# Kernel tuning notes

Measured on AMD Instinct MI355X. Metric: run time of the kernel, lower is better.

Reference implementation:

```python
import jax, jax.numpy as jnp
import numpy as np

# dims: C=d_model, DI=expand*C (d_inner), S=d_state, R=dt_rank, K=4 scan dirs
C, DI, S, R, K = 64, 128, 16, 4, 4
Hh, Ww, T, Bsz = 48, 48, 4, 1

def _silu(x):
    return x * jax.nn.sigmoid(x)

def _ln_c(x, w, b, eps=1e-6):
    # LayerNorm2d: normalize over channel dim of [B,C,H,W]
    mu = jnp.mean(x, axis=1, keepdims=True)
    var = jnp.var(x, axis=1, keepdims=True)
    return (x - mu) * jax.lax.rsqrt(var + eps) * w[None, :, None, None] + b[None, :, None, None]

def _cal_kl(cur, prev):
    # elementwise KL over channel-softmax distributions, shape-preserving
    lp = jax.nn.log_softmax(prev, axis=1)
    lq = jax.nn.log_softmax(cur, axis=1)
    return jnp.exp(lp) * (lp - lq)

def _ss2d(x, in_w, in_b, cw, cb, xp_w, dt_w, dt_b, A_logs, Ds, onw, onb, ow, ob):
    # VMamba-style SS2D, channel-first input [B,C,H,W]
    B_, _, H_, W_ = x.shape
    L = H_ * W_
    xz = jnp.einsum('dc,bchw->bdhw', in_w, x) + in_b[None, :, None, None]
    xc, z = jnp.split(xz, 2, axis=1)
    di = xc.shape[1]
    xc = jax.lax.conv_general_dilated(xc, cw[:, None], (1, 1), 'SAME',
        dimension_numbers=('NCHW', 'OIHW', 'NCHW'), feature_group_count=di)
    xc = _silu(xc + cb[None, :, None, None])
    # cross-scan: row-major, col-major, and their reverses -> [B,K,DI,L]
    x1 = xc.reshape(B_, di, L)
    x2 = jnp.swapaxes(xc, 2, 3).reshape(B_, di, L)
    xs = jnp.stack([x1, x2, jnp.flip(x1, -1), jnp.flip(x2, -1)], axis=1)
    xdbl = jnp.einsum('krd,bkdl->bkrl', xp_w, xs)
    dts, Bs, Cs = jnp.split(xdbl, [R, R + S], axis=2)  # [B,K,R,L],[B,K,S,L],[B,K,S,L]
    dt = jax.nn.softplus(jnp.einsum('kdr,bkrl->bkdl', dt_w, dts) + dt_b[None, :, :, None])
    A = -jnp.exp(A_logs)  # [K,DI,S]
    dA = jnp.exp(dt[..., None] * A[None, :, :, None, :])                    # [B,K,DI,L,S]
    dBx = (dt * xs)[..., None] * jnp.swapaxes(Bs, 2, 3)[:, :, None, :, :]   # [B,K,DI,L,S]
    def comb(e1, e2):
        a1, b1 = e1
        a2, b2 = e2
        return (a1 * a2, a2 * b1 + b2)
    _, hs = jax.lax.associative_scan(comb, (dA, dBx), axis=3)
    y = jnp.einsum('bkdls,bksl->bkdl', hs, Cs) + Ds[None, :, :, None] * xs
    # cross-merge back to row-major and sum
    y0 = y[:, 0]
    y1 = jnp.swapaxes(y[:, 1].reshape(B_, di, W_, H_), 2, 3).reshape(B_, di, L)
    y2 = jnp.flip(y[:, 2], -1)
    y3 = jnp.swapaxes(jnp.flip(y[:, 3], -1).reshape(B_, di, W_, H_), 2, 3).reshape(B_, di, L)
    yy = (y0 + y1 + y2 + y3).reshape(B_, di, H_, W_)
    yy = _ln_c(yy, onw, onb) * _silu(z)
    return jnp.einsum('cd,bdhw->bchw', ow, yy) + ob[None, :, None, None]

def setup_inputs():
    key = jax.random.key(0)
    ks = jax.random.split(key, 16)
    rn = lambda k, shp, s: jax.random.normal(k, shp, jnp.float32) * s
    return {
        'image_sequence': rn(ks[0], (Bsz, T, C, Hh, Ww), 1.0),
        'difficult_zone': rn(ks[1], (Bsz, C, Hh, Ww), 1.0),
        'sigma': rn(ks[2], (Bsz, C, Hh, Ww), 0.1),
        # params stacked over the 2 SS2D modules: [0]=mamba_sigma, [1]=mamba_bias
        'in_w': rn(ks[3], (2, 2 * DI, C), C ** -0.5),
        'in_b': rn(ks[4], (2, 2 * DI), 0.02),
        'conv_w': rn(ks[5], (2, DI, 3, 3), 1.0 / 3.0),
        'conv_b': rn(ks[6], (2, DI), 0.02),
        'xp_w': rn(ks[7], (2, K, R + 2 * S, DI), DI ** -0.5),
        'dt_w': rn(ks[8], (2, K, DI, R), R ** -0.5),
        'dt_b': rn(ks[9], (2, K, DI), 0.5),
        'A_logs': jnp.log(1.0 + jax.random.uniform(ks[10], (2, K, DI, S), jnp.float32)),
        'Ds': rn(ks[11], (2, K, DI), 0.5),
        'onw': jnp.ones((2, DI), jnp.float32),
        'onb': jnp.zeros((2, DI), jnp.float32),
        'ow': rn(ks[12], (2, C, DI), 0.02),
        'ob': jnp.zeros((2, C), jnp.float32),
        'niw': jnp.ones((C,), jnp.float32),
        'nib': jnp.zeros((C,), jnp.float32),
        'ndw': jnp.ones((C,), jnp.float32),
        'ndb': jnp.zeros((C,), jnp.float32),
    }

def reference(image_sequence, difficult_zone, sigma, in_w, in_b, conv_w, conv_b, xp_w, dt_w, dt_b, A_logs, Ds, onw, onb, ow, ob, niw, nib, ndw, ndb):
    prev = _ln_c(difficult_zone, ndw, ndb)
    cur = prev * jnp.exp(sigma)  # prev / exp(-sigma)
    for t in range(T):  # strictly sequential recurrence over `length` steps
        s = _ss2d(_cal_kl(cur, prev), in_w[0], in_b[0], conv_w[0], conv_b[0], xp_w[0],
                  dt_w[0], dt_b[0], A_logs[0], Ds[0], onw[0], onb[0], ow[0], ob[0])
        bias = _ss2d(_ln_c(image_sequence[:, t], niw, nib), in_w[1], in_b[1], conv_w[1], conv_b[1], xp_w[1],
                     dt_w[1], dt_b[1], A_logs[1], Ds[1], onw[1], onb[1], ow[1], ob[1])
        cur, prev = cur * jnp.exp(s) + bias, cur
    return cur
```

## Files before the change

kernel.cpp:

```cpp
#include <hip/hip_runtime.h>

#define DEV __device__ __forceinline__

constexpr int Cc = 64, DIc = 128, Sc = 16, Rc = 4, Kc = 4;
constexpr int Lc = 2304, Tc = 4;
constexpr int NCH = 144, CHL = 16;

constexpr int OFF_XCPRE = 0;
constexpr int OFF_Z     = 294912;
constexpr int OFF_XACT  = 589824;
constexpr int OFF_DTS   = 884736;
constexpr int OFF_BS    = 921600;
constexpr int OFF_CS    = 1069056;
constexpr int OFF_Y     = 1216512;
constexpr int OFF_SUMA  = 2396160;
constexpr int OFF_SUMB  = 3575808;
constexpr int OFF_H0    = 4755456;
constexpr int SLOTF     = 5935104;
constexpr int OFF_B1    = 5 * SLOTF;
constexpr int OFF_B2    = OFF_B1 + Lc * Cc;
constexpr int OFF_BIAS  = OFF_B2 + Lc * Cc;
constexpr int OFF_TW    = OFF_BIAS + Tc * Lc * Cc;
constexpr int TW_INW  = 0;
constexpr int TW_XPW  = 32768;
constexpr int TW_OW   = 69632;
constexpr int TW_CW   = 86016;
constexpr int TW_AT   = 88320;
constexpr int TW_DTW  = 104704;

struct Params {
  const float *img, *dz, *sigma, *in_w, *in_b, *conv_w, *conv_b, *xp_w, *dt_w,
              *dt_b, *A_logs, *Ds, *onw, *onb, *ow, *ob, *niw, *nib, *ndw, *ndb;
  float* outp;
  float* ws;
};

DEV float wsum(float v) {
#pragma unroll
  for (int m = 32; m; m >>= 1) v += __shfl_xor(v, m, 64);
  return v;
}
DEV float wmax(float v) {
#pragma unroll
  for (int m = 32; m; m >>= 1) v = fmaxf(v, __shfl_xor(v, m, 64));
  return v;
}
DEV float sigmoidf(float x) { return 1.f / (1.f + __expf(-x)); }
DEV float softplusf(float v) { return (v > 20.f) ? v : __logf(1.f + __expf(v)); }
DEV float fexp2(float x) { return __builtin_amdgcn_exp2f(x); }

DEV int perm_idx(int k, int l) {
  if (k == 0) return l;
  if (k == 1) return (l % 48) * 48 + l / 48;
  if (k == 2) return Lc - 1 - l;
  int pp = Lc - 1 - l;
  return (pp % 48) * 48 + pp / 48;
}

DEV int perm_stride(int k) {
  return (k == 0) ? 1 : (k == 1) ? 48 : (k == 2) ? -1 : -48;
}

__global__ __launch_bounds__(256) void g_transpose(Params p) {
  float* tw = p.ws + OFF_TW;
  int i = blockIdx.x * 256 + threadIdx.x;
  if (i < 32768) {
    int d = i & 255, cc = (i >> 8) & 63, b = i >> 14;
    tw[TW_INW + i] = p.in_w[(b * 256 + d) * 64 + cc];
  }
  if (i < 36864) {
    int kr = i % 144, cc = (i / 144) & 127, b = i / (144 * 128);
    tw[TW_XPW + i] = p.xp_w[(b * 144 + kr) * 128 + cc];
  }
  if (i < 16384) {
    int c = i & 63, d = (i >> 6) & 127, b = i >> 13;
    tw[TW_OW + i] = p.ow[(b * 64 + c) * 128 + d];
  }
  if (i < 2304) {
    int d = i & 127, kk = (i >> 7) % 9, b = i / 1152;
    tw[TW_CW + i] = p.conv_w[(b * 128 + d) * 9 + kk];
  }
  if (i < 16384) {
    int d = i & 127, bks = i >> 7;
    int s = bks & 15, bk = bks >> 4;
    tw[TW_AT + i] = -__expf(p.A_logs[(bk * 128 + d) * 16 + s]) * 1.4426950408889634f;
  }
  if (i < 4096) {
    int d = i & 127, bkr = i >> 7;
    int r = bkr & 3, bk = bkr >> 2;
    tw[TW_DTW + i] = p.dt_w[(bk * 128 + d) * 4 + r];
  }
}

__global__ __launch_bounds__(256) void g_inproj(Params p) {
  __shared__ float xv[8][64];
  int tid = threadIdx.x;
  int slot = blockIdx.y;
  int branch = (slot >= 4) ? 0 : 1;
  float* ws = p.ws;
  float* base = ws + (size_t)slot * SLOTF;
  float* xcpre = base + OFF_XCPRE;
  float* zbuf  = base + OFF_Z;
  const float* wT = ws + OFF_TW + TW_INW + branch * 64 * 256;
  int l0 = blockIdx.x * 8;
  int wv = tid >> 6, c = tid & 63;
#pragma unroll
  for (int q = 0; q < 2; q++) {
    int pp = wv * 2 + q;
    int l = l0 + pp;
    float x;
    if (branch == 1) {
      float v = p.img[(slot * Cc + c) * Lc + l];
      float mu = wsum(v) * (1.f / 64.f);
      float var = wsum(v * v) * (1.f / 64.f) - mu * mu;
      x = (v - mu) * rsqrtf(var + 1e-6f) * p.niw[c] + p.nib[c];
    } else {
      float v = p.dz[c * Lc + l];
      float mu = wsum(v) * (1.f / 64.f);
      float var = wsum(v * v) * (1.f / 64.f) - mu * mu;
      float pv = (v - mu) * rsqrtf(var + 1e-6f) * p.ndw[c] + p.ndb[c];
      float cv = pv * __expf(p.sigma[c * Lc + l]);
      (ws + OFF_B1)[l * Cc + c] = cv;
      float mp = wmax(pv);
      float sp = wsum(__expf(pv - mp));
      float lp = pv - mp - __logf(sp);
      float mq = wmax(cv);
      float sq = wsum(__expf(cv - mq));
      float lq = cv - mq - __logf(sq);
      x = __expf(lp) * (lp - lq);
    }
    xv[pp][c] = x;
  }
  __syncthreads();
  int d = tid;
  float acc[8];
#pragma unroll
  for (int q = 0; q < 8; q++) acc[q] = 0.f;
  for (int cc = 0; cc < Cc; cc++) {
    float wval = wT[cc * 256 + d];
#pragma unroll
    for (int q = 0; q < 8; q++) acc[q] += wval * xv[q][cc];
  }
  float bv = p.in_b[branch * 2 * DIc + d];
  if (d < DIc) {
#pragma unroll
    for (int q = 0; q < 8; q++) xcpre[(l0 + q) * DIc + d] = acc[q] + bv;
  } else {
    int dd = d - DIc;
#pragma unroll
    for (int q = 0; q < 8; q++) zbuf[(l0 + q) * DIc + dd] = acc[q] + bv;
  }
}

__global__ __launch_bounds__(256) void g_conv(Params p, int slot_base) {
  __shared__ float xv[4][DIc];
  int tid = threadIdx.x;
  int slot = slot_base + blockIdx.y;
  int branch = (slot >= 4) ? 0 : 1;
  float* ws = p.ws;
  float* base = ws + (size_t)slot * SLOTF;
  float* xcpre = base + OFF_XCPRE;
  float* xact  = base + OFF_XACT;
  float* dtsb  = base + OFF_DTS;
  float* Bsb   = base + OFF_BS;
  float* Csb   = base + OFF_CS;
  const float* cwT  = ws + OFF_TW + TW_CW + branch * 9 * 128;
  const float* xpwT = ws + OFF_TW + TW_XPW + branch * 128 * 144;
  int h = blockIdx.x / 12;
  int w0 = (blockIdx.x % 12) * 4;
  for (int it = tid; it < 4 * DIc; it += 256) {
    int d = it & (DIc - 1);
    int pp = it >> 7;
    int w = w0 + pp;
    float acc = 0.f;
#pragma unroll
    for (int kh = 0; kh < 3; kh++) {
      int hh = h + kh - 1;
      if ((unsigned)hh < 48u) {
#pragma unroll
        for (int kw = 0; kw < 3; kw++) {
          int wp = w + kw - 1;
          if ((unsigned)wp < 48u)
            acc += cwT[(kh * 3 + kw) * 128 + d] * xcpre[(hh * 48 + wp) * DIc + d];
        }
      }
    }
    float v = acc + p.conv_b[branch * DIc + d];
    float s = v * sigmoidf(v);
    xv[pp][d] = s;
    xact[(h * 48 + w) * DIc + d] = s;
  }
  __syncthreads();
  if (tid < Kc * 36) {
    int k = tid / 36, r = tid % 36;
    float acc[4] = {0.f, 0.f, 0.f, 0.f};
    for (int cc = 0; cc < DIc; cc++) {
      float wvv = xpwT[cc * 144 + tid];
#pragma unroll
      for (int pp = 0; pp < 4; pp++) acc[pp] += wvv * xv[pp][cc];
    }
#pragma unroll
    for (int pp = 0; pp < 4; pp++) {
      int w = w0 + pp;
      int lr = h * 48 + w, lcx = w * 48 + h;
      int pos = (k == 0) ? lr : (k == 1) ? lcx : (k == 2) ? (Lc - 1 - lr) : (Lc - 1 - lcx);
      if (r < Rc) dtsb[(k * Lc + pos) * Rc + r] = acc[pp];
      else if (r < Rc + Sc) Bsb[(k * Lc + pos) * Sc + (r - Rc)] = acc[pp];
      else Csb[(k * Lc + pos) * Sc + (r - Rc - Sc)] = acc[pp];
    }
  }
}

__global__ __launch_bounds__(256, 4) void g_scan1(Params p, int slot_base) {
  __shared__ alignas(16) float2 sDt[CHL][DIc];
  __shared__ alignas(16) float sB[CHL * Sc];
  __shared__ float sCT[2][DIc];
  int tid = threadIdx.x;
  int slot = slot_base + blockIdx.y;
  int branch = (slot >= 4) ? 0 : 1;
  float* ws = p.ws;
  float* base = ws + (size_t)slot * SLOTF;
  const float* xact = base + OFF_XACT;
  const float* Bsb  = base + OFF_BS;
  const float* dtsb = base + OFF_DTS;
  float* sumA = base + OFF_SUMA;
  float* sumB = base + OFF_SUMB;
  int bx = blockIdx.x;
  int k = bx / NCH, ch = bx - k * NCH;
  int d = tid & (DIc - 1);
  int sh = tid >> 7;
  int bk = branch * Kc + k;
  const float* AT   = ws + OFF_TW + TW_AT;
  const float* dtwT = ws + OFF_TW + TW_DTW;
  int l0 = ch * CHL;
  sB[tid] = Bsb[(k * Lc + l0) * Sc + tid];
  float A2[8];
#pragma unroll
  for (int j = 0; j < 8; j++) A2[j] = AT[(bk * 16 + sh * 8 + j) * 128 + d];
  int idx0 = perm_idx(k, l0);
  int st = perm_stride(k);
  float xw[8];
#pragma unroll
  for (int j = 0; j < 8; j++) xw[j] = xact[(idx0 + st * (sh * 8 + j)) * DIc + d];
  float4 dtq[8];
#pragma unroll
  for (int j = 0; j < 8; j++)
    dtq[j] = *(const float4*)(dtsb + (size_t)(k * Lc + l0 + sh * 8 + j) * 4);
  float dw0 = dtwT[(bk * 4 + 0) * 128 + d];
  float dw1 = dtwT[(bk * 4 + 1) * 128 + d];
  float dw2 = dtwT[(bk * 4 + 2) * 128 + d];
  float dw3 = dtwT[(bk * 4 + 3) * 128 + d];
  float db = p.dt_b[bk * DIc + d];
  float ct = 0.f;
#pragma unroll
  for (int j = 0; j < 8; j++) {
    float v = db + dw0 * dtq[j].x + dw1 * dtq[j].y + dw2 * dtq[j].z + dw3 * dtq[j].w;
    float dtv = softplusf(v);
    sDt[sh * 8 + j][d] = make_float2(dtv, dtv * xw[j]);
    ct += dtv;
  }
  sCT[sh][d] = ct;
  __syncthreads();
  float CT = sCT[0][d] + sCT[1][d];
  const float4* B4 = (const float4*)sB;
  float h0 = 0.f, h1 = 0.f, h2 = 0.f, h3 = 0.f, h4 = 0.f, h5 = 0.f, h6 = 0.f, h7 = 0.f;
#pragma unroll
  for (int ib = 0; ib < 4; ib++) {
    float2 dg[4];
    float4 Bg0[4], Bg1[4];
#pragma unroll
    for (int q = 0; q < 4; q++) {
      int i = ib * 4 + q;
      dg[q]  = sDt[i][d];
      Bg0[q] = B4[i * 4 + sh * 2];
      Bg1[q] = B4[i * 4 + sh * 2 + 1];
    }
#pragma unroll
    for (int q = 0; q < 4; q++) {
      float dtv = dg[q].x, dtx = dg[q].y;
#define STEP1(hh, bb, aa2) { float da = fexp2(dtv * (aa2)); hh = da * hh + dtx * (bb); }
      STEP1(h0, Bg0[q].x, A2[0]);
      STEP1(h1, Bg0[q].y, A2[1]);
      STEP1(h2, Bg0[q].z, A2[2]);
      STEP1(h3, Bg0[q].w, A2[3]);
      STEP1(h4, Bg1[q].x, A2[4]);
      STEP1(h5, Bg1[q].y, A2[5]);
      STEP1(h6, Bg1[q].z, A2[6]);
      STEP1(h7, Bg1[q].w, A2[7]);
#undef STEP1
    }
  }
  float* sa = sumA + ((size_t)(k * NCH + ch) * Sc + sh * 8) * DIc + d;
  float* sb = sumB + ((size_t)(k * NCH + ch) * Sc + sh * 8) * DIc + d;
#pragma unroll
  for (int j = 0; j < 8; j++) sa[j * DIc] = fexp2(A2[j] * CT);
  sb[0 * DIc] = h0; sb[1 * DIc] = h1; sb[2 * DIc] = h2; sb[3 * DIc] = h3;
  sb[4 * DIc] = h4; sb[5 * DIc] = h5; sb[6 * DIc] = h6; sb[7 * DIc] = h7;
}

__global__ __launch_bounds__(256) void g_mid(Params p, int slot_base) {
  int gid = blockIdx.x * 256 + threadIdx.x;
  int slot = slot_base + blockIdx.y;
  float* base = p.ws + (size_t)slot * SLOTF;
  const float* sumA = base + OFF_SUMA;
  const float* sumB = base + OFF_SUMB;
  float* h0 = base + OFF_H0;
  int d = gid & (DIc - 1);
  int s = (gid >> 7) & (Sc - 1);
  int k = gid >> 11;
  float h = 0.f;
  for (int g = 0; g < NCH / 16; g++) {
    float a[16], b[16];
#pragma unroll
    for (int j = 0; j < 16; j++) {
      int idx = ((k * NCH + g * 16 + j) * Sc + s) * DIc + d;
      a[j] = sumA[idx];
      b[j] = sumB[idx];
    }
#pragma unroll
    for (int j = 0; j < 16; j++) {
      int idx = ((k * NCH + g * 16 + j) * Sc + s) * DIc + d;
      h0[idx] = h;
      h = a[j] * h + b[j];
    }
  }
}

__global__ __launch_bounds__(512, 4) void g_scan2(Params p, int slot_base) {
  __shared__ alignas(16) float2 sDt[2][CHL][DIc];
  __shared__ alignas(16) float sB[2][CHL * Sc];
  __shared__ alignas(16) float sC[2][CHL * Sc];
  int tid = threadIdx.x;
  int slot = slot_base + blockIdx.y;
  int branch = (slot >= 4) ? 0 : 1;
  float* ws = p.ws;
  float* base = ws + (size_t)slot * SLOTF;
  const float* xact = base + OFF_XACT;
  const float* Bsb  = base + OFF_BS;
  const float* Csb  = base + OFF_CS;
  const float* dtsb = base + OFF_DTS;
  const float* h0b  = base + OFF_H0;
  int pair = blockIdx.x / NCH, chA = blockIdx.x - pair * NCH;
  int d = tid & (DIc - 1);
  int sh = (tid >> 7) & 1;
  int dir = tid >> 8;
  int k = pair + 2 * dir;
  int ch = dir ? (NCH - 1 - chA) : chA;
  int bk = branch * Kc + k;
  float* ypair = base + OFF_Y + (size_t)pair * Lc * DIc;
  const float* AT   = ws + OFF_TW + TW_AT;
  const float* dtwT = ws + OFF_TW + TW_DTW;
  int l0 = ch * CHL;
  int t8 = tid & 255;
  sB[dir][t8] = Bsb[(k * Lc + l0) * Sc + t8];
  sC[dir][t8] = Csb[(k * Lc + l0) * Sc + t8];
  float A2[8];
#pragma unroll
  for (int j = 0; j < 8; j++) A2[j] = AT[(bk * 16 + sh * 8 + j) * 128 + d];
  float hr0, hr1, hr2, hr3, hr4, hr5, hr6, hr7;
  {
    const float* hp = h0b + ((size_t)(k * NCH + ch) * Sc + sh * 8) * DIc + d;
    hr0 = hp[0 * DIc]; hr1 = hp[1 * DIc]; hr2 = hp[2 * DIc]; hr3 = hp[3 * DIc];
    hr4 = hp[4 * DIc]; hr5 = hp[5 * DIc]; hr6 = hp[6 * DIc]; hr7 = hp[7 * DIc];
  }
  int idx0 = perm_idx(k, l0);
  int st = perm_stride(k);
  float xw[8];
#pragma unroll
  for (int j = 0; j < 8; j++) xw[j] = xact[(idx0 + st * (sh * 8 + j)) * DIc + d];
  float4 dtq[8];
#pragma unroll
  for (int j = 0; j < 8; j++)
    dtq[j] = *(const float4*)(dtsb + (size_t)(k * Lc + l0 + sh * 8 + j) * 4);
  float dw0 = dtwT[(bk * 4 + 0) * 128 + d];
  float dw1 = dtwT[(bk * 4 + 1) * 128 + d];
  float dw2 = dtwT[(bk * 4 + 2) * 128 + d];
  float dw3 = dtwT[(bk * 4 + 3) * 128 + d];
  float db = p.dt_b[bk * DIc + d];
  float Dv = p.Ds[bk * DIc + d];
#pragma unroll
  for (int j = 0; j < 8; j++) {
    float v = db + dw0 * dtq[j].x + dw1 * dtq[j].y + dw2 * dtq[j].z + dw3 * dtq[j].w;
    float dtv = softplusf(v);
    sDt[dir][sh * 8 + j][d] = make_float2(dtv, dtv * xw[j]);
  }
  __syncthreads();
  const float4* B4 = (const float4*)sB[dir];
  const float4* C4 = (const float4*)sC[dir];
  float acc[CHL];
#pragma unroll
  for (int ib = 0; ib < 4; ib++) {
    float2 dg[4];
    float4 Bg0[4], Bg1[4];
#pragma unroll
    for (int q = 0; q < 4; q++) {
      int i = ib * 4 + q;
      dg[q]  = sDt[dir][i][d];
      Bg0[q] = B4[i * 4 + sh * 2];
      Bg1[q] = B4[i * 4 + sh * 2 + 1];
    }
#pragma unroll
    for (int q = 0; q < 4; q++) {
      int i = ib * 4 + q;
      float4 Cg0 = C4[i * 4 + sh * 2];
      float4 Cg1 = C4[i * 4 + sh * 2 + 1];
      float dtv = dg[q].x, dtx = dg[q].y;
      float a = 0.f;
#define STEP(hh, bb, cc, aa2) { float da = fexp2(dtv * (aa2)); hh = da * hh + dtx * (bb); a += hh * (cc); }
      STEP(hr0, Bg0[q].x, Cg0.x, A2[0]);
      STEP(hr1, Bg0[q].y, Cg0.y, A2[1]);
      STEP(hr2, Bg0[q].z, Cg0.z, A2[2]);
      STEP(hr3, Bg0[q].w, Cg0.w, A2[3]);
      STEP(hr4, Bg1[q].x, Cg1.x, A2[4]);
      STEP(hr5, Bg1[q].y, Cg1.y, A2[5]);
      STEP(hr6, Bg1[q].z, Cg1.z, A2[6]);
      STEP(hr7, Bg1[q].w, Cg1.w, A2[7]);
#undef STEP
      acc[i] = a;
    }
  }
  if (sh == 0) {
#pragma unroll
    for (int j = 0; j < 8; j++) acc[j] += Dv * xw[j];
  } else {
#pragma unroll
    for (int j = 0; j < 8; j++) acc[8 + j] += Dv * xw[j];
  }
  __syncthreads();
  float* yred = (float*)sDt;
  if (sh == 1) {
#pragma unroll
    for (int i = 0; i < CHL; i++) yred[(dir * CHL + i) * DIc + d] = acc[i];
  }
  __syncthreads();
  if (sh == 0 && dir == 1) {
#pragma unroll
    for (int i = 0; i < CHL; i++) yred[(CHL + i) * DIc + d] += acc[i];
  }
  __syncthreads();
  if (sh == 0 && dir == 0) {
#pragma unroll
    for (int i = 0; i < CHL; i++)
      ypair[(size_t)(idx0 + st * i) * DIc + d] =
          acc[i] + yred[i * DIc + d] + yred[(CHL + (CHL - 1 - i)) * DIc + d];
  }
}

__global__ __launch_bounds__(256) void g_out_bias(Params p) {
  __shared__ float yy[4][DIc];
  __shared__ float ml[4][DIc];
  __shared__ float mnv[4], isv[4];
  int tid = threadIdx.x;
  int slot = blockIdx.y;
  float* ws = p.ws;
  float* base = ws + (size_t)slot * SLOTF;
  const float* y01 = base + OFF_Y;
  const float* y23 = base + OFF_Y + Lc * DIc;
  const float* zb = base + OFF_Z;
  const float* owT = ws + OFF_TW + TW_OW + 128 * 64;
  float* biasb = ws + OFF_BIAS;
  int l0 = blockIdx.x * 4;
  for (int it = tid; it < 4 * DIc; it += 256) {
    int d = it & (DIc - 1), pp = it >> 7;
    size_t off = (size_t)(l0 + pp) * DIc + d;
    yy[pp][d] = y01[off] + y23[off];
  }
  __syncthreads();
  {
    int wv = tid >> 6, c = tid & 63;
    float a = yy[wv][c], b = yy[wv][c + 64];
    float s1 = wsum(a + b);
    float s2 = wsum(a * a + b * b);
    float mu = s1 * (1.f / 128.f);
    float var = s2 * (1.f / 128.f) - mu * mu;
    if (c == 0) { mnv[wv] = mu; isv[wv] = rsqrtf(var + 1e-6f); }
  }
  __syncthreads();
  for (int it = tid; it < 4 * DIc; it += 256) {
    int d = it & (DIc - 1), pp = it >> 7;
    int l = l0 + pp;
    float m = (yy[pp][d] - mnv[pp]) * isv[pp] * p.onw[DIc + d] + p.onb[DIc + d];
    float zv = zb[l * DIc + d];
    ml[pp][d] = m * zv * sigmoidf(zv);
  }
  __syncthreads();
  {
    int pp = tid >> 6, c = tid & 63;
    int l = l0 + pp;
    float acc = p.ob[Cc + c];
    for (int d2 = 0; d2 < DIc; d2++) acc += owT[d2 * 64 + c] * ml[pp][d2];
    biasb[(slot * Lc + l) * Cc + c] = acc;
  }
}

__global__ __launch_bounds__(256) void g_out_s(Params p, int targ, int fuse, int finalw,
                                               const float* curb, float* nxtb) {
  __shared__ float yy[4][DIc];
  __shared__ float ml[4][DIc];
  __shared__ float xvs[4][64];
  __shared__ float mnv[4], isv[4];
  int tid = threadIdx.x;
  float* ws = p.ws;
  float* base = ws + (size_t)4 * SLOTF;
  const float* y01 = base + OFF_Y;
  const float* y23 = base + OFF_Y + Lc * DIc;
  const float* zb = base + OFF_Z;
  float* xcpre = base + OFF_XCPRE;
  float* zbuf  = base + OFF_Z;
  const float* owT  = ws + OFF_TW + TW_OW;
  const float* inwT = ws + OFF_TW + TW_INW;
  const float* biasb = ws + OFF_BIAS;
  int l0 = blockIdx.x * 4;
  for (int it = tid; it < 4 * DIc; it += 256) {
    int d = it & (DIc - 1), pp = it >> 7;
    size_t off = (size_t)(l0 + pp) * DIc + d;
    yy[pp][d] = y01[off] + y23[off];
  }
  __syncthreads();
  {
    int wv = tid >> 6, c = tid & 63;
    float a = yy[wv][c], b = yy[wv][c + 64];
    float s1 = wsum(a + b);
    float s2 = wsum(a * a + b * b);
    float mu = s1 * (1.f / 128.f);
    float var = s2 * (1.f / 128.f) - mu * mu;
    if (c == 0) { mnv[wv] = mu; isv[wv] = rsqrtf(var + 1e-6f); }
  }
  __syncthreads();
  for (int it = tid; it < 4 * DIc; it += 256) {
    int d = it & (DIc - 1), pp = it >> 7;
    int l = l0 + pp;
    float m = (yy[pp][d] - mnv[pp]) * isv[pp] * p.onw[d] + p.onb[d];
    float zv = zb[l * DIc + d];
    ml[pp][d] = m * zv * sigmoidf(zv);
  }
  __syncthreads();
  {
    int pp = tid >> 6, c = tid & 63;
    int l = l0 + pp;
    float acc = p.ob[c];
    for (int d2 = 0; d2 < DIc; d2++) acc += owT[d2 * 64 + c] * ml[pp][d2];
    float cv = curb[l * Cc + c];
    float nv = cv * __expf(acc) + biasb[(targ * Lc + l) * Cc + c];
    nxtb[l * Cc + c] = nv;
    if (finalw) p.outp[c * Lc + l] = nv;
    if (fuse) {
      float mp = wmax(cv);
      float sp = wsum(__expf(cv - mp));
      float lp = cv - mp - __logf(sp);
      float mq = wmax(nv);
      float sq = wsum(__expf(nv - mq));
      float lq = nv - mq - __logf(sq);
      xvs[pp][c] = __expf(lp) * (lp - lq);
    }
  }
  if (fuse) {
    __syncthreads();
    int d = tid;
    float acc[4] = {0.f, 0.f, 0.f, 0.f};
    for (int cc = 0; cc < Cc; cc++) {
      float wval = inwT[cc * 256 + d];
#pragma unroll
      for (int pp = 0; pp < 4; pp++) acc[pp] += wval * xvs[pp][cc];
    }
    float bv = p.in_b[d];
    if (d < DIc) {
#pragma unroll
      for (int pp = 0; pp < 4; pp++) xcpre[(l0 + pp) * DIc + d] = acc[pp] + bv;
    } else {
      int dd = d - DIc;
#pragma unroll
      for (int pp = 0; pp < 4; pp++) zbuf[(l0 + pp) * DIc + dd] = acc[pp] + bv;
    }
  }
}

extern "C" void kernel_launch(void* const* d_in, const int* in_sizes, int n_in,
                              void* d_out, int out_size, void* d_ws, size_t ws_size,
                              hipStream_t stream) {
  (void)in_sizes; (void)n_in; (void)out_size; (void)ws_size;
  Params p;
  p.img    = (const float*)d_in[0];
  p.dz     = (const float*)d_in[1];
  p.sigma  = (const float*)d_in[2];
  p.in_w   = (const float*)d_in[3];
  p.in_b   = (const float*)d_in[4];
  p.conv_w = (const float*)d_in[5];
  p.conv_b = (const float*)d_in[6];
  p.xp_w   = (const float*)d_in[7];
  p.dt_w   = (const float*)d_in[8];
  p.dt_b   = (const float*)d_in[9];
  p.A_logs = (const float*)d_in[10];
  p.Ds     = (const float*)d_in[11];
  p.onw    = (const float*)d_in[12];
  p.onb    = (const float*)d_in[13];
  p.ow     = (const float*)d_in[14];
  p.ob     = (const float*)d_in[15];
  p.niw    = (const float*)d_in[16];
  p.nib    = (const float*)d_in[17];
  p.ndw    = (const float*)d_in[18];
  p.ndb    = (const float*)d_in[19];
  p.outp   = (float*)d_out;
  p.ws     = (float*)d_ws;


  hipLaunchKernelGGL(g_transpose, dim3(144), dim3(256), 0, stream, p);
  hipLaunchKernelGGL(g_inproj, dim3(288, 5), dim3(256), 0, stream, p);
  hipLaunchKernelGGL(g_conv, dim3(576, 5), dim3(256), 0, stream, p, 0);
  hipLaunchKernelGGL(g_scan1, dim3(Kc * NCH, 5), dim3(256), 0, stream, p, 0);
  hipLaunchKernelGGL(g_mid, dim3(32, 5), dim3(256), 0, stream, p, 0);
  hipLaunchKernelGGL(g_scan2, dim3(2 * NCH, 5), dim3(512), 0, stream, p, 0);
  hipLaunchKernelGGL(g_out_bias, dim3(576, 4), dim3(256), 0, stream, p);

  float* b1 = p.ws + OFF_B1;
  float* b2 = p.ws + OFF_B2;
  hipLaunchKernelGGL(g_out_s, dim3(576), dim3(256), 0, stream, p, 0, 1, 0,
                     (const float*)b1, b2);
  for (int t = 1; t < Tc; t++) {
    const float* curb = (t & 1) ? b2 : b1;
    float* nxtb       = (t & 1) ? b1 : b2;
    hipLaunchKernelGGL(g_conv, dim3(576, 1), dim3(256), 0, stream, p, 4);
    hipLaunchKernelGGL(g_scan1, dim3(Kc * NCH, 1), dim3(256), 0, stream, p, 4);
    hipLaunchKernelGGL(g_mid, dim3(32, 1), dim3(256), 0, stream, p, 4);
    hipLaunchKernelGGL(g_scan2, dim3(2 * NCH, 1), dim3(512), 0, stream, p, 4);
    hipLaunchKernelGGL(g_out_s, dim3(576), dim3(256), 0, stream, p,
                       t, (t == Tc - 1) ? 0 : 1, (t == Tc - 1) ? 1 : 0, curb, nxtb);
  }
}
```

Baseline: 404.7 us.

## Compute dt per thread in scan kernels and split scan2 blocks by channel halves

In both chunked scan kernels each thread now computes softplus(dt) and dt*x for all 16 chunk positions in registers. Previously the two state-halves shared this work through a shared-memory staging array. scan2 also changes from 512-thread blocks covering all 128 channels to 256-thread blocks covering 64 channels, which doubles the grid and shrinks the shared-memory reduction buffer. The aim is to cut shared-memory traffic and make blocks smaller so more can be resident, at the cost of redundant dt computation and global loads, plus higher register pressure from the per-thread arrays.

```diff
diff --git a/kernel.cpp b/kernel.cpp
--- a/kernel.cpp
+++ b/kernel.cpp
@@ -212,9 +212,7 @@
 }
 
 __global__ __launch_bounds__(256, 4) void g_scan1(Params p, int slot_base) {
-  __shared__ alignas(16) float2 sDt[CHL][DIc];
   __shared__ alignas(16) float sB[CHL * Sc];
-  __shared__ float sCT[2][DIc];
   int tid = threadIdx.x;
   int slot = slot_base + blockIdx.y;
   int branch = (slot >= 4) ? 0 : 1;
@@ -237,65 +235,51 @@
   float A2[8];
 #pragma unroll
   for (int j = 0; j < 8; j++) A2[j] = AT[(bk * 16 + sh * 8 + j) * 128 + d];
-  int idx0 = perm_idx(k, l0);
-  int st = perm_stride(k);
-  float xw[8];
-#pragma unroll
-  for (int j = 0; j < 8; j++) xw[j] = xact[(idx0 + st * (sh * 8 + j)) * DIc + d];
-  float4 dtq[8];
-#pragma unroll
-  for (int j = 0; j < 8; j++)
-    dtq[j] = *(const float4*)(dtsb + (size_t)(k * Lc + l0 + sh * 8 + j) * 4);
   float dw0 = dtwT[(bk * 4 + 0) * 128 + d];
   float dw1 = dtwT[(bk * 4 + 1) * 128 + d];
   float dw2 = dtwT[(bk * 4 + 2) * 128 + d];
   float dw3 = dtwT[(bk * 4 + 3) * 128 + d];
   float db = p.dt_b[bk * DIc + d];
-  float ct = 0.f;
-#pragma unroll
-  for (int j = 0; j < 8; j++) {
-    float v = db + dw0 * dtq[j].x + dw1 * dtq[j].y + dw2 * dtq[j].z + dw3 * dtq[j].w;
-    float dtv = softplusf(v);
-    sDt[sh * 8 + j][d] = make_float2(dtv, dtv * xw[j]);
-    ct += dtv;
-  }
-  sCT[sh][d] = ct;
-  __syncthreads();
-  float CT = sCT[0][d] + sCT[1][d];
+  int idx0 = perm_idx(k, l0);
+  int st = perm_stride(k);
+  float dtv[CHL], dtx[CHL];
+  float CT = 0.f;
+#pragma unroll
+  for (int i = 0; i < CHL; i++) {
+    float4 dt4 = *(const float4*)(dtsb + (size_t)(k * Lc + l0 + i) * 4);
+    float v = db + dw0 * dt4.x + dw1 * dt4.y + dw2 * dt4.z + dw3 * dt4.w;
+    float t = softplusf(v);
+    dtv[i] = t;
+    dtx[i] = t * xact[(idx0 + st * i) * DIc + d];
+    CT += t;
+  }
+  __syncthreads();
   const float4* B4 = (const float4*)sB;
-  float h0 = 0.f, h1 = 0.f, h2 = 0.f, h3 = 0.f, h4 = 0.f, h5 = 0.f, h6 = 0.f, h7 = 0.f;
-#pragma unroll
-  for (int ib = 0; ib < 4; ib++) {
-    float2 dg[4];
-    float4 Bg0[4], Bg1[4];
-#pragma unroll
-    for (int q = 0; q < 4; q++) {
-      int i = ib * 4 + q;
-      dg[q]  = sDt[i][d];
-      Bg0[q] = B4[i * 4 + sh * 2];
-      Bg1[q] = B4[i * 4 + sh * 2 + 1];
-    }
-#pragma unroll
-    for (int q = 0; q < 4; q++) {
-      float dtv = dg[q].x, dtx = dg[q].y;
-#define STEP1(hh, bb, aa2) { float da = fexp2(dtv * (aa2)); hh = da * hh + dtx * (bb); }
-      STEP1(h0, Bg0[q].x, A2[0]);
-      STEP1(h1, Bg0[q].y, A2[1]);
-      STEP1(h2, Bg0[q].z, A2[2]);
-      STEP1(h3, Bg0[q].w, A2[3]);
-      STEP1(h4, Bg1[q].x, A2[4]);
-      STEP1(h5, Bg1[q].y, A2[5]);
-      STEP1(h6, Bg1[q].z, A2[6]);
-      STEP1(h7, Bg1[q].w, A2[7]);
+  float h[8];
+#pragma unroll
+  for (int j = 0; j < 8; j++) h[j] = 0.f;
+#pragma unroll
+  for (int i = 0; i < CHL; i++) {
+    float4 Bg0 = B4[i * 4 + sh * 2];
+    float4 Bg1 = B4[i * 4 + sh * 2 + 1];
+    float t = dtv[i], tx = dtx[i];
+#define STEP1(hh, bb, aa2) { float da = fexp2(t * (aa2)); hh = da * hh + tx * (bb); }
+    STEP1(h[0], Bg0.x, A2[0]);
+    STEP1(h[1], Bg0.y, A2[1]);
+    STEP1(h[2], Bg0.z, A2[2]);
+    STEP1(h[3], Bg0.w, A2[3]);
+    STEP1(h[4], Bg1.x, A2[4]);
+    STEP1(h[5], Bg1.y, A2[5]);
+    STEP1(h[6], Bg1.z, A2[6]);
+    STEP1(h[7], Bg1.w, A2[7]);
 #undef STEP1
-    }
   }
   float* sa = sumA + ((size_t)(k * NCH + ch) * Sc + sh * 8) * DIc + d;
   float* sb = sumB + ((size_t)(k * NCH + ch) * Sc + sh * 8) * DIc + d;
 #pragma unroll
   for (int j = 0; j < 8; j++) sa[j * DIc] = fexp2(A2[j] * CT);
-  sb[0 * DIc] = h0; sb[1 * DIc] = h1; sb[2 * DIc] = h2; sb[3 * DIc] = h3;
-  sb[4 * DIc] = h4; sb[5 * DIc] = h5; sb[6 * DIc] = h6; sb[7 * DIc] = h7;
+#pragma unroll
+  for (int j = 0; j < 8; j++) sb[j * DIc] = h[j];
 }
 
 __global__ __launch_bounds__(256) void g_mid(Params p, int slot_base) {
@@ -326,10 +310,10 @@
   }
 }
 
-__global__ __launch_bounds__(512, 4) void g_scan2(Params p, int slot_base) {
-  __shared__ alignas(16) float2 sDt[2][CHL][DIc];
+__global__ __launch_bounds__(256, 4) void g_scan2(Params p, int slot_base) {
   __shared__ alignas(16) float sB[2][CHL * Sc];
   __shared__ alignas(16) float sC[2][CHL * Sc];
+  __shared__ alignas(16) float yred[2][CHL][64];
   int tid = threadIdx.x;
   int slot = slot_base + blockIdx.y;
   int branch = (slot >= 4) ? 0 : 1;
@@ -340,109 +324,94 @@
   const float* Csb  = base + OFF_CS;
   const float* dtsb = base + OFF_DTS;
   const float* h0b  = base + OFF_H0;
-  int pair = blockIdx.x / NCH, chA = blockIdx.x - pair * NCH;
-  int d = tid & (DIc - 1);
-  int sh = (tid >> 7) & 1;
-  int dir = tid >> 8;
-  int k = pair + 2 * dir;
+  int bx = blockIdx.x;
+  int pair = bx / (2 * NCH);
+  int rem = bx - pair * 2 * NCH;
+  int chA = rem >> 1;
+  int dblk = rem & 1;
+  int dm = tid & 63;
+  int d = dblk * 64 + dm;
+  int sh = (tid >> 6) & 1;
+  int dir = tid >> 7;
+  int kA = pair, kB = pair + 2;
+  int l0A = chA * CHL, l0B = (NCH - 1 - chA) * CHL;
+  sB[0][tid] = Bsb[(kA * Lc + l0A) * Sc + tid];
+  sB[1][tid] = Bsb[(kB * Lc + l0B) * Sc + tid];
+  sC[0][tid] = Csb[(kA * Lc + l0A) * Sc + tid];
+  sC[1][tid] = Csb[(kB * Lc + l0B) * Sc + tid];
+  int k = dir ? kB : kA;
   int ch = dir ? (NCH - 1 - chA) : chA;
   int bk = branch * Kc + k;
   float* ypair = base + OFF_Y + (size_t)pair * Lc * DIc;
   const float* AT   = ws + OFF_TW + TW_AT;
   const float* dtwT = ws + OFF_TW + TW_DTW;
   int l0 = ch * CHL;
-  int t8 = tid & 255;
-  sB[dir][t8] = Bsb[(k * Lc + l0) * Sc + t8];
-  sC[dir][t8] = Csb[(k * Lc + l0) * Sc + t8];
   float A2[8];
 #pragma unroll
   for (int j = 0; j < 8; j++) A2[j] = AT[(bk * 16 + sh * 8 + j) * 128 + d];
-  float hr0, hr1, hr2, hr3, hr4, hr5, hr6, hr7;
+  float h[8];
   {
     const float* hp = h0b + ((size_t)(k * NCH + ch) * Sc + sh * 8) * DIc + d;
-    hr0 = hp[0 * DIc]; hr1 = hp[1 * DIc]; hr2 = hp[2 * DIc]; hr3 = hp[3 * DIc];
-    hr4 = hp[4 * DIc]; hr5 = hp[5 * DIc]; hr6 = hp[6 * DIc]; hr7 = hp[7 * DIc];
-  }
-  int idx0 = perm_idx(k, l0);
-  int st = perm_stride(k);
-  float xw[8];
-#pragma unroll
-  for (int j = 0; j < 8; j++) xw[j] = xact[(idx0 + st * (sh * 8 + j)) * DIc + d];
-  float4 dtq[8];
-#pragma unroll
-  for (int j = 0; j < 8; j++)
-    dtq[j] = *(const float4*)(dtsb + (size_t)(k * Lc + l0 + sh * 8 + j) * 4);
+#pragma unroll
+    for (int j = 0; j < 8; j++) h[j] = hp[j * DIc];
+  }
   float dw0 = dtwT[(bk * 4 + 0) * 128 + d];
   float dw1 = dtwT[(bk * 4 + 1) * 128 + d];
   float dw2 = dtwT[(bk * 4 + 2) * 128 + d];
   float dw3 = dtwT[(bk * 4 + 3) * 128 + d];
   float db = p.dt_b[bk * DIc + d];
   float Dv = p.Ds[bk * DIc + d];
-#pragma unroll
-  for (int j = 0; j < 8; j++) {
-    float v = db + dw0 * dtq[j].x + dw1 * dtq[j].y + dw2 * dtq[j].z + dw3 * dtq[j].w;
-    float dtv = softplusf(v);
-    sDt[dir][sh * 8 + j][d] = make_float2(dtv, dtv * xw[j]);
+  int idx0 = perm_idx(k, l0);
+  int st = perm_stride(k);
+  float dtv[CHL], dtx[CHL], acc[CHL];
+#pragma unroll
+  for (int i = 0; i < CHL; i++) {
+    float4 dt4 = *(const float4*)(dtsb + (size_t)(k * Lc + l0 + i) * 4);
+    float v = db + dw0 * dt4.x + dw1 * dt4.y + dw2 * dt4.z + dw3 * dt4.w;
+    float t = softplusf(v);
+    float xv = xact[(idx0 + st * i) * DIc + d];
+    dtv[i] = t;
+    dtx[i] = t * xv;
+    acc[i] = (sh == 0) ? Dv * xv : 0.f;
   }
   __syncthreads();
   const float4* B4 = (const float4*)sB[dir];
   const float4* C4 = (const float4*)sC[dir];
-  float acc[CHL];
-#pragma unroll
-  for (int ib = 0; ib < 4; ib++) {
-    float2 dg[4];
-    float4 Bg0[4], Bg1[4];
-#pragma unroll
-    for (int q = 0; q < 4; q++) {
-      int i = ib * 4 + q;
-      dg[q]  = sDt[dir][i][d];
-      Bg0[q] = B4[i * 4 + sh * 2];
-      Bg1[q] = B4[i * 4 + sh * 2 + 1];
-    }
-#pragma unroll
-    for (int q = 0; q < 4; q++) {
-      int i = ib * 4 + q;
-      float4 Cg0 = C4[i * 4 + sh * 2];
-      float4 Cg1 = C4[i * 4 + sh * 2 + 1];
-      float dtv = dg[q].x, dtx = dg[q].y;
-      float a = 0.f;
-#define STEP(hh, bb, cc, aa2) { float da = fexp2(dtv * (aa2)); hh = da * hh + dtx * (bb); a += hh * (cc); }
-      STEP(hr0, Bg0[q].x, Cg0.x, A2[0]);
-      STEP(hr1, Bg0[q].y, Cg0.y, A2[1]);
-      STEP(hr2, Bg0[q].z, Cg0.z, A2[2]);
-      STEP(hr3, Bg0[q].w, Cg0.w, A2[3]);
-      STEP(hr4, Bg1[q].x, Cg1.x, A2[4]);
-      STEP(hr5, Bg1[q].y, Cg1.y, A2[5]);
-      STEP(hr6, Bg1[q].z, Cg1.z, A2[6]);
-      STEP(hr7, Bg1[q].w, Cg1.w, A2[7]);
+#pragma unroll
+  for (int i = 0; i < CHL; i++) {
+    float4 Bg0 = B4[i * 4 + sh * 2];
+    float4 Bg1 = B4[i * 4 + sh * 2 + 1];
+    float4 Cg0 = C4[i * 4 + sh * 2];
+    float4 Cg1 = C4[i * 4 + sh * 2 + 1];
+    float t = dtv[i], tx = dtx[i];
+    float a = acc[i];
+#define STEP(hh, bb, cc, aa2) { float da = fexp2(t * (aa2)); hh = da * hh + tx * (bb); a += hh * (cc); }
+    STEP(h[0], Bg0.x, Cg0.x, A2[0]);
+    STEP(h[1], Bg0.y, Cg0.y, A2[1]);
+    STEP(h[2], Bg0.z, Cg0.z, A2[2]);
+    STEP(h[3], Bg0.w, Cg0.w, A2[3]);
+    STEP(h[4], Bg1.x, Cg1.x, A2[4]);
+    STEP(h[5], Bg1.y, Cg1.y, A2[5]);
+    STEP(h[6], Bg1.z, Cg1.z, A2[6]);
+    STEP(h[7], Bg1.w, Cg1.w, A2[7]);
 #undef STEP
-      acc[i] = a;
-    }
-  }
+    acc[i] = a;
+  }
+  if (sh == 1) {
+#pragma unroll
+    for (int i = 0; i < CHL; i++) yred[dir][i][dm] = acc[i];
+  }
+  __syncthreads();
   if (sh == 0) {
 #pragma unroll
-    for (int j = 0; j < 8; j++) acc[j] += Dv * xw[j];
-  } else {
-#pragma unroll
-    for (int j = 0; j < 8; j++) acc[8 + j] += Dv * xw[j];
-  }
-  __syncthreads();
-  float* yred = (float*)sDt;
-  if (sh == 1) {
-#pragma unroll
-    for (int i = 0; i < CHL; i++) yred[(dir * CHL + i) * DIc + d] = acc[i];
-  }
-  __syncthreads();
-  if (sh == 0 && dir == 1) {
-#pragma unroll
-    for (int i = 0; i < CHL; i++) yred[(CHL + i) * DIc + d] += acc[i];
+    for (int i = 0; i < CHL; i++) yred[dir][i][dm] += acc[i];
   }
   __syncthreads();
   if (sh == 0 && dir == 0) {
 #pragma unroll
     for (int i = 0; i < CHL; i++)
       ypair[(size_t)(idx0 + st * i) * DIc + d] =
-          acc[i] + yred[i * DIc + d] + yred[(CHL + (CHL - 1 - i)) * DIc + d];
+          yred[0][i][dm] + yred[1][CHL - 1 - i][dm];
   }
 }
 
@@ -609,7 +578,7 @@
   hipLaunchKernelGGL(g_conv, dim3(576, 5), dim3(256), 0, stream, p, 0);
   hipLaunchKernelGGL(g_scan1, dim3(Kc * NCH, 5), dim3(256), 0, stream, p, 0);
   hipLaunchKernelGGL(g_mid, dim3(32, 5), dim3(256), 0, stream, p, 0);
-  hipLaunchKernelGGL(g_scan2, dim3(2 * NCH, 5), dim3(512), 0, stream, p, 0);
+  hipLaunchKernelGGL(g_scan2, dim3(2 * NCH * 2, 5), dim3(256), 0, stream, p, 0);
   hipLaunchKernelGGL(g_out_bias, dim3(576, 4), dim3(256), 0, stream, p);
 
   float* b1 = p.ws + OFF_B1;
@@ -622,7 +591,7 @@
     hipLaunchKernelGGL(g_conv, dim3(576, 1), dim3(256), 0, stream, p, 4);
     hipLaunchKernelGGL(g_scan1, dim3(Kc * NCH, 1), dim3(256), 0, stream, p, 4);
     hipLaunchKernelGGL(g_mid, dim3(32, 1), dim3(256), 0, stream, p, 4);
-    hipLaunchKernelGGL(g_scan2, dim3(2 * NCH, 1), dim3(512), 0, stream, p, 4);
+    hipLaunchKernelGGL(g_scan2, dim3(2 * NCH * 2, 1), dim3(256), 0, stream, p, 4);
     hipLaunchKernelGGL(g_out_s, dim3(576), dim3(256), 0, stream, p,
                        t, (t == Tc - 1) ? 0 : 1, (t == Tc - 1) ? 1 : 0, curb, nxtb);
   }
```

Result: faster. 389.5 us (-3.7%).
